# Performance work log

Measured on AMD Instinct MI355X. Metric: run time of the kernel, lower is better.

Reference implementation:

```python
import jax, jax.numpy as jnp
import numpy as np

DEFAULT_MASK_VALUE = -0.7 * float(np.finfo(np.float32).max)


def setup_inputs() -> dict:
    key = jax.random.key(0)
    kq, kk, kv = jax.random.split(key, 3)
    B, S, Hq, Hkv, D = 2, 2048, 16, 8, 128
    return {
        "query": jax.random.normal(kq, (B, S, Hq, D), dtype=jnp.float32),
        "key": jax.random.normal(kk, (B, S, Hkv, D), dtype=jnp.float32),
        "value": jax.random.normal(kv, (B, S, Hkv, D), dtype=jnp.float32),
        "chunk_size": 512,
    }


def reference(query, key, value, chunk_size):
    """Chunked-causal GQA attention (AttentionOp with attention_type='chunk').

    Tokens attend only within their own chunk, causally. This is exactly the
    mask from _generate_chunk_attention_mask, exploited as a block-diagonal
    structure so cross-chunk logits are never materialized.
    """
    B, S, Hq, D = query.shape
    Hkv = key.shape[2]
    G = Hq // Hkv  # GQA group size
    C = int(chunk_size)
    NC = S // C
    scale = 1.0 / np.float32(np.sqrt(D))  # depth scaling (folded into query init in MaxText)

    # float32 qk product / logits (float32_qk_product & float32_logits = True)
    qf = query.astype(jnp.float32).reshape(B, NC, C, Hkv, G, D)
    kf = key.astype(jnp.float32).reshape(B, NC, C, Hkv, D)
    vf = value.reshape(B, NC, C, Hkv, D)

    # per-chunk logits: [B, NC, Hkv, G, C(q), C(k)]
    logits = jnp.einsum("bnqhgd,bnkhd->bnhgqk", qf, kf) * scale

    # causal mask within each chunk (apply_mask_to_logits semantics)
    causal = jnp.arange(C)[:, None] >= jnp.arange(C)[None, :]
    logits = jnp.where(causal, logits, DEFAULT_MASK_VALUE)

    probs = jax.nn.softmax(logits, axis=-1).astype(value.dtype)
    out = jnp.einsum("bnhgqk,bnkhd->bnqhgd", probs, vf)
    return out.reshape(B, S, Hq, D)
```

## Files before the change

kernel.cpp:

```cpp
#include <hip/hip_runtime.h>
#include <hip/hip_bf16.h>

typedef __bf16 bf16;
typedef bf16  bf16x2 __attribute__((ext_vector_type(2)));
typedef bf16  bf16x4 __attribute__((ext_vector_type(4)));
typedef bf16  bf16x8 __attribute__((ext_vector_type(8)));
typedef float f32x4  __attribute__((ext_vector_type(4)));
typedef float f32x16 __attribute__((ext_vector_type(16)));

#define MFMA32(A, B, C) __builtin_amdgcn_mfma_f32_32x32x16_bf16((A), (B), (C), 0, 0, 0)

namespace {
constexpr int   kS = 2048, kHq = 16, kHkv = 8, kD = 128, kChunk = 512;
constexpr int   kNT   = 8;
constexpr int   kStrK = kHkv * kD;
constexpr float kScale = 0.08838834764831845f;
constexpr float kThr   = 8.0f;
}

union U32B { bf16x2 h; unsigned u; };
union PAU  { unsigned u[4]; bf16x8 v; };

__global__ __launch_bounds__(512, 2)
void attn_chunk(const float* __restrict__ Qg, const float* __restrict__ Kg,
                const float* __restrict__ Vg, float* __restrict__ Og) {
  __shared__ __attribute__((aligned(16))) bf16 ldsK[2][64 * 128];
  __shared__ __attribute__((aligned(16))) bf16 ldsV[2][128 * 64];

  const int t = threadIdx.x, lane = t & 63, w = t >> 6;
  const int l31 = lane & 31, hi = lane >> 5;

  const int bid = blockIdx.x;
  const int gid = (bid & 7) * 32 + (bid >> 3);
  const int p = gid & 1, hq = (gid >> 1) & 15, n = (gid >> 5) & 3, b = (gid >> 7) & 1;
  const int h = hq >> 1;

  const int a     = (w < 4) ? (7 - 2 * w) : (2 * w - 8);
  const int need  = a + 1;
  const int strip = 2 * a + p;
  const int qg    = n * kChunk + strip * 32 + l31;
  const int rowoff = 32 * p + l31;

  bf16x8 qf[8];
  {
    const float* qp = Qg + ((size_t)(b * kS + qg) * kHq + hq) * kD;
#pragma unroll
    for (int dk = 0; dk < 8; ++dk) {
      f32x4 x0 = *(const f32x4*)(qp + dk * 16 + 8 * hi);
      f32x4 x1 = *(const f32x4*)(qp + dk * 16 + 8 * hi + 4);
      bf16x8 v;
#pragma unroll
      for (int j = 0; j < 4; ++j) { v[j] = (bf16)(x0[j] * kScale); v[4 + j] = (bf16)(x1[j] * kScale); }
      qf[dk] = v;
    }
  }

  f32x16 o[4];
#pragma unroll
  for (int dt = 0; dt < 4; ++dt)
#pragma unroll
    for (int r = 0; r < 16; ++r) o[dt][r] = 0.f;
  float m = -1e30f, l = 0.f;

  const float* kpz = Kg + ((size_t)(b * kS + n * kChunk) * kHkv + h) * kD;
  const float* vpz = Vg + ((size_t)(b * kS + n * kChunk) * kHkv + h) * kD;

  const int sKey = t >> 5, sD4 = t & 31;
  const int vKp = t & 31, vD4h = t >> 5;

  f32x4 kf[4], va[2], vb[2];
  auto issue = [&](int kt) {
    const float* kp = kpz + (size_t)kt * 64 * kStrK;
    const float* vp = vpz + (size_t)kt * 64 * kStrK;
#pragma unroll
    for (int it = 0; it < 4; ++it)
      kf[it] = *(const f32x4*)(kp + (size_t)(16 * it + sKey) * kStrK + sD4 * 4);
#pragma unroll
    for (int it = 0; it < 2; ++it) {
      va[it] = *(const f32x4*)(vp + (size_t)(2 * vKp) * kStrK + (16 * it + vD4h) * 4);
      vb[it] = *(const f32x4*)(vp + (size_t)(2 * vKp + 1) * kStrK + (16 * it + vD4h) * 4);
    }
  };
  auto stage = [&](int buf) {
#pragma unroll
    for (int it = 0; it < 4; ++it) {
      const int key = 16 * it + sKey;
      bf16x4 kb;
#pragma unroll
      for (int j = 0; j < 4; ++j) kb[j] = (bf16)kf[it][j];
      *(bf16x4*)&ldsK[buf][key * 128 + ((sD4 * 4) ^ ((key & 7) << 3))] = kb;
    }
#pragma unroll
    for (int it = 0; it < 2; ++it) {
#pragma unroll
      for (int j = 0; j < 4; ++j) {
        const int d = (16 * it + vD4h) * 4 + j;
        U32B uu; uu.h = bf16x2{(bf16)va[it][j], (bf16)vb[it][j]};
        *(unsigned*)&ldsV[buf][d * 64 + ((2 * vKp) ^ ((d & 7) << 3))] = uu.u;
      }
    }
  };

  auto compute = [&](int buf, bool diag) {
    f32x16 s[2];
#pragma unroll
    for (int ks = 0; ks < 2; ++ks)
#pragma unroll
      for (int r = 0; r < 16; ++r) s[ks][r] = 0.f;
    __builtin_amdgcn_s_setprio(1);
#pragma unroll
    for (int ks = 0; ks < 2; ++ks) {
      const int key = ks * 32 + l31, swz = (key & 7) << 3;
      const bf16* kb = &ldsK[buf][key * 128];
#pragma unroll
      for (int dk = 0; dk < 8; ++dk) {
        bf16x8 kfr = *(const bf16x8*)&kb[(dk * 16 + 8 * hi) ^ swz];
        s[ks] = MFMA32(kfr, qf[dk], s[ks]);
      }
    }
    __builtin_amdgcn_s_setprio(0);
    if (diag) {
#pragma unroll
      for (int ks = 0; ks < 2; ++ks)
#pragma unroll
        for (int r = 0; r < 16; ++r) {
          const int key = ks * 32 + (r & 3) + 8 * (r >> 2) + 4 * hi;
          if (key > rowoff) s[ks][r] = -1e30f;
        }
    }
    float mx = -1e30f;
#pragma unroll
    for (int ks = 0; ks < 2; ++ks)
#pragma unroll
      for (int r = 0; r < 16; ++r) mx = fmaxf(mx, s[ks][r]);
    mx = fmaxf(mx, __shfl_xor(mx, 32, 64));
    if (__any(mx > m + kThr)) {
      const float mn = fmaxf(m, mx), c = __expf(m - mn);
      l *= c;
#pragma unroll
      for (int dt = 0; dt < 4; ++dt)
#pragma unroll
        for (int r = 0; r < 16; ++r) o[dt][r] *= c;
      m = mn;
    }
    unsigned u[2][8];
    float lp = 0.f;
#pragma unroll
    for (int ks = 0; ks < 2; ++ks)
#pragma unroll
      for (int j = 0; j < 8; ++j) {
        const float p0 = __expf(s[ks][2 * j] - m), p1 = __expf(s[ks][2 * j + 1] - m);
        lp += p0 + p1;
        U32B uu; uu.h = bf16x2{(bf16)p0, (bf16)p1};
        u[ks][j] = uu.u;
      }
    l += lp;
    unsigned rc[2][4];
#pragma unroll
    for (int ks = 0; ks < 2; ++ks)
#pragma unroll
      for (int i = 0; i < 4; ++i)
        rc[ks][i] = (unsigned)__shfl_xor((int)u[ks][(i & 1) + 4 * (i >> 1) + (hi ? 0 : 2)], 32, 64);
    bf16x8 pa[4];
#pragma unroll
    for (int ks = 0; ks < 2; ++ks)
#pragma unroll
      for (int kh = 0; kh < 2; ++kh) {
        PAU pu;
        pu.u[0] = hi ? rc[ks][2 * kh]     : u[ks][4 * kh];
        pu.u[1] = hi ? rc[ks][2 * kh + 1] : u[ks][4 * kh + 1];
        pu.u[2] = hi ? u[ks][4 * kh + 2]  : rc[ks][2 * kh];
        pu.u[3] = hi ? u[ks][4 * kh + 3]  : rc[ks][2 * kh + 1];
        pa[ks * 2 + kh] = pu.v;
      }
    __builtin_amdgcn_s_setprio(1);
#pragma unroll
    for (int dt = 0; dt < 4; ++dt) {
      const int d = dt * 32 + l31, swz = (d & 7) << 3;
      const bf16* vbp = &ldsV[buf][d * 64];
#pragma unroll
      for (int ksl = 0; ksl < 4; ++ksl) {
        bf16x8 vfr = *(const bf16x8*)&vbp[(ksl * 16 + 8 * hi) ^ swz];
        o[dt] = MFMA32(vfr, pa[ksl], o[dt]);
      }
    }
    __builtin_amdgcn_s_setprio(0);
  };

  issue(0);
  stage(0);
  issue(1);
  __syncthreads();
#pragma unroll 1
  for (int kt = 0; kt < kNT; ++kt) {
    if (kt + 1 < kNT) {
      stage((kt + 1) & 1);
      if (kt + 2 < kNT) issue(kt + 2);
    }
    if (kt < need) compute(kt & 1, kt == need - 1);
    if (kt + 1 < kNT) __syncthreads();
  }

  l += __shfl_xor(l, 32, 64);
  const float inv = 1.f / l;
  float* op = Og + ((size_t)(b * kS + qg) * kHq + hq) * kD;
#pragma unroll
  for (int dt = 0; dt < 4; ++dt)
#pragma unroll
    for (int rq = 0; rq < 4; ++rq) {
      f32x4 st;
#pragma unroll
      for (int rr = 0; rr < 4; ++rr) st[rr] = o[dt][4 * rq + rr] * inv;
      *(f32x4*)(op + dt * 32 + 8 * rq + 4 * hi) = st;
    }
}

extern "C" void kernel_launch(void* const* d_in, const int* in_sizes, int n_in,
                              void* d_out, int out_size, void* d_ws, size_t ws_size,
                              hipStream_t stream) {
  (void)in_sizes; (void)n_in; (void)d_ws; (void)ws_size; (void)out_size;
  const float* Q = (const float*)d_in[0];
  const float* K = (const float*)d_in[1];
  const float* V = (const float*)d_in[2];
  float* O = (float*)d_out;
  dim3 grid(256);
  dim3 block(512);
  hipLaunchKernelGGL(attn_chunk, grid, block, 0, stream, Q, K, V, O);
}
```

Baseline: 34.96 us.

## Split chunk work into 4-wave blocks with per-block loop bounds and exp2 softmax

Each block now has 4 waves instead of 8, with twice as many blocks. Strips are paired so each block's K/V loop only runs to the deepest strip it needs (maxNeed), which cuts K/V tile loads for blocks whose strips sit early in the chunk. The log2e factor is folded into the query scale so the softmax can use exp2 directly. The plain barrier is replaced by an explicit lgkmcnt wait plus s_barrier. In exchange, each thread issues twice the K/V loads per tile, and K/V is now loaded by four blocks per chunk and head instead of two.

```diff
diff --git a/kernel.cpp b/kernel.cpp
--- a/kernel.cpp
+++ b/kernel.cpp
@@ -12,16 +12,23 @@
 
 namespace {
 constexpr int   kS = 2048, kHq = 16, kHkv = 8, kD = 128, kChunk = 512;
-constexpr int   kNT   = 8;
-constexpr int   kStrK = kHkv * kD;
-constexpr float kScale = 0.08838834764831845f;
-constexpr float kThr   = 8.0f;
+constexpr int   kStrK  = kHkv * kD;
+constexpr float kLog2e = 1.4426950408889634f;
+constexpr float kScale = 0.08838834764831845f * kLog2e;
+constexpr float kThr   = 8.0f * kLog2e;
 }
 
 union U32B { bf16x2 h; unsigned u; };
 union PAU  { unsigned u[4]; bf16x8 v; };
 
-__global__ __launch_bounds__(512, 2)
+__device__ __forceinline__ void lgkm_barrier() {
+  __builtin_amdgcn_sched_barrier(0);
+  asm volatile("s_waitcnt lgkmcnt(0)" ::: "memory");
+  __builtin_amdgcn_s_barrier();
+  __builtin_amdgcn_sched_barrier(0);
+}
+
+__global__ __launch_bounds__(256, 2)
 void attn_chunk(const float* __restrict__ Qg, const float* __restrict__ Kg,
                 const float* __restrict__ Vg, float* __restrict__ Og) {
   __shared__ __attribute__((aligned(16))) bf16 ldsK[2][64 * 128];
@@ -31,15 +38,15 @@
   const int l31 = lane & 31, hi = lane >> 5;
 
   const int bid = blockIdx.x;
-  const int gid = (bid & 7) * 32 + (bid >> 3);
-  const int p = gid & 1, hq = (gid >> 1) & 15, n = (gid >> 5) & 3, b = (gid >> 7) & 1;
+  const int gid = (bid & 7) * 64 + (bid >> 3);
+  const int j = gid & 3, hq = (gid >> 2) & 15, n = (gid >> 6) & 3, b = (gid >> 8) & 1;
   const int h = hq >> 1;
 
-  const int a     = (w < 4) ? (7 - 2 * w) : (2 * w - 8);
-  const int need  = a + 1;
-  const int strip = 2 * a + p;
-  const int qg    = n * kChunk + strip * 32 + l31;
-  const int rowoff = 32 * p + l31;
+  const int strip   = (w == 0) ? j : (w == 1) ? (15 - j) : (w == 2) ? (7 - j) : (8 + j);
+  const int need    = (strip >> 1) + 1;
+  const int maxNeed = 8 - (j >> 1);
+  const int qg      = n * kChunk + strip * 32 + l31;
+  const int rowoff  = 32 * (strip & 1) + l31;
 
   bf16x8 qf[8];
   {
@@ -50,7 +57,7 @@
       f32x4 x1 = *(const f32x4*)(qp + dk * 16 + 8 * hi + 4);
       bf16x8 v;
 #pragma unroll
-      for (int j = 0; j < 4; ++j) { v[j] = (bf16)(x0[j] * kScale); v[4 + j] = (bf16)(x1[j] * kScale); }
+      for (int q = 0; q < 4; ++q) { v[q] = (bf16)(x0[q] * kScale); v[4 + q] = (bf16)(x1[q] * kScale); }
       qf[dk] = v;
     }
   }
@@ -68,34 +75,34 @@
   const int sKey = t >> 5, sD4 = t & 31;
   const int vKp = t & 31, vD4h = t >> 5;
 
-  f32x4 kf[4], va[2], vb[2];
+  f32x4 kf[8], va[4], vb[4];
   auto issue = [&](int kt) {
     const float* kp = kpz + (size_t)kt * 64 * kStrK;
     const float* vp = vpz + (size_t)kt * 64 * kStrK;
 #pragma unroll
-    for (int it = 0; it < 4; ++it)
-      kf[it] = *(const f32x4*)(kp + (size_t)(16 * it + sKey) * kStrK + sD4 * 4);
-#pragma unroll
-    for (int it = 0; it < 2; ++it) {
-      va[it] = *(const f32x4*)(vp + (size_t)(2 * vKp) * kStrK + (16 * it + vD4h) * 4);
-      vb[it] = *(const f32x4*)(vp + (size_t)(2 * vKp + 1) * kStrK + (16 * it + vD4h) * 4);
+    for (int it = 0; it < 8; ++it)
+      kf[it] = *(const f32x4*)(kp + (size_t)(8 * it + sKey) * kStrK + sD4 * 4);
+#pragma unroll
+    for (int it = 0; it < 4; ++it) {
+      va[it] = *(const f32x4*)(vp + (size_t)(2 * vKp) * kStrK + (8 * it + vD4h) * 4);
+      vb[it] = *(const f32x4*)(vp + (size_t)(2 * vKp + 1) * kStrK + (8 * it + vD4h) * 4);
     }
   };
   auto stage = [&](int buf) {
 #pragma unroll
+    for (int it = 0; it < 8; ++it) {
+      const int key = 8 * it + sKey;
+      bf16x4 kb;
+#pragma unroll
+      for (int q = 0; q < 4; ++q) kb[q] = (bf16)kf[it][q];
+      *(bf16x4*)&ldsK[buf][key * 128 + ((sD4 * 4) ^ ((key & 7) << 3))] = kb;
+    }
+#pragma unroll
     for (int it = 0; it < 4; ++it) {
-      const int key = 16 * it + sKey;
-      bf16x4 kb;
-#pragma unroll
-      for (int j = 0; j < 4; ++j) kb[j] = (bf16)kf[it][j];
-      *(bf16x4*)&ldsK[buf][key * 128 + ((sD4 * 4) ^ ((key & 7) << 3))] = kb;
-    }
-#pragma unroll
-    for (int it = 0; it < 2; ++it) {
-#pragma unroll
-      for (int j = 0; j < 4; ++j) {
-        const int d = (16 * it + vD4h) * 4 + j;
-        U32B uu; uu.h = bf16x2{(bf16)va[it][j], (bf16)vb[it][j]};
+#pragma unroll
+      for (int q = 0; q < 4; ++q) {
+        const int d = (8 * it + vD4h) * 4 + q;
+        U32B uu; uu.h = bf16x2{(bf16)va[it][q], (bf16)vb[it][q]};
         *(unsigned*)&ldsV[buf][d * 64 + ((2 * vKp) ^ ((d & 7) << 3))] = uu.u;
       }
     }
@@ -135,7 +142,7 @@
       for (int r = 0; r < 16; ++r) mx = fmaxf(mx, s[ks][r]);
     mx = fmaxf(mx, __shfl_xor(mx, 32, 64));
     if (__any(mx > m + kThr)) {
-      const float mn = fmaxf(m, mx), c = __expf(m - mn);
+      const float mn = fmaxf(m, mx), c = exp2f(m - mn);
       l *= c;
 #pragma unroll
       for (int dt = 0; dt < 4; ++dt)
@@ -148,11 +155,11 @@
 #pragma unroll
     for (int ks = 0; ks < 2; ++ks)
 #pragma unroll
-      for (int j = 0; j < 8; ++j) {
-        const float p0 = __expf(s[ks][2 * j] - m), p1 = __expf(s[ks][2 * j + 1] - m);
+      for (int q = 0; q < 8; ++q) {
+        const float p0 = exp2f(s[ks][2 * q] - m), p1 = exp2f(s[ks][2 * q + 1] - m);
         lp += p0 + p1;
         U32B uu; uu.h = bf16x2{(bf16)p0, (bf16)p1};
-        u[ks][j] = uu.u;
+        u[ks][q] = uu.u;
       }
     l += lp;
     unsigned rc[2][4];
@@ -190,15 +197,15 @@
   issue(0);
   stage(0);
   issue(1);
-  __syncthreads();
+  lgkm_barrier();
 #pragma unroll 1
-  for (int kt = 0; kt < kNT; ++kt) {
-    if (kt + 1 < kNT) {
+  for (int kt = 0; kt < maxNeed; ++kt) {
+    if (kt + 1 < maxNeed) {
       stage((kt + 1) & 1);
-      if (kt + 2 < kNT) issue(kt + 2);
-    }
-    if (kt < need) compute(kt & 1, kt == need - 1);
-    if (kt + 1 < kNT) __syncthreads();
+      if (kt + 2 < maxNeed) issue(kt + 2);
+    }
+    if (kt < need) compute(kt & 1, kt + 1 == need);
+    if (kt + 1 < maxNeed) lgkm_barrier();
   }
 
   l += __shfl_xor(l, 32, 64);
@@ -223,7 +230,7 @@
   const float* K = (const float*)d_in[1];
   const float* V = (const float*)d_in[2];
   float* O = (float*)d_out;
-  dim3 grid(256);
-  dim3 block(512);
+  dim3 grid(512);
+  dim3 block(256);
   hipLaunchKernelGGL(attn_chunk, grid, block, 0, stream, Q, K, V, O);
 }
```

New measurement: 45.54 us. +30.2%, slower.

## Prepack K/V to bf16 MFMA-fragment layout in workspace, stream from global

Applied to the files above, without the earlier changes.

Adds a prepack kernel that converts K and V to bf16 once per call and writes them in a tiled layout matching the MFMA fragment order. The attention kernel then reads fragments straight from global/L2 without LDS staging or barriers, and skips tiles beyond its causal limit. This removes redundant fp32 loads and conversions done by every query-head block, at the cost of a second launch and a workspace round trip. The softmax also switches to exp2 with log2e folded into the scale, and an LDS-based fallback kernel runs when the workspace is too small.

```diff
diff --git a/kernel.cpp b/kernel.cpp
--- a/kernel.cpp
+++ b/kernel.cpp
@@ -12,21 +12,70 @@
 
 namespace {
 constexpr int   kS = 2048, kHq = 16, kHkv = 8, kD = 128, kChunk = 512;
-constexpr int   kNT   = 8;
-constexpr int   kStrK = kHkv * kD;
-constexpr float kScale = 0.08838834764831845f;
-constexpr float kThr   = 8.0f;
+constexpr int   kStrK  = kHkv * kD;
+constexpr float kLog2e = 1.4426950408889634f;
+constexpr float kScale = 0.08838834764831845f * kLog2e;
+constexpr float kThr   = 8.0f * kLog2e;
+constexpr size_t kWsNeed = 512ull * 8192 * 2 * 2;
 }
 
 union U32B { bf16x2 h; unsigned u; };
 union PAU  { unsigned u[4]; bf16x8 v; };
 
+__global__ __launch_bounds__(256, 4)
+void prepack(const float* __restrict__ Kg, const float* __restrict__ Vg,
+             bf16* __restrict__ Kws, bf16* __restrict__ Vws) {
+  __shared__ __attribute__((aligned(16))) bf16 img[8192];
+  const int t  = threadIdx.x;
+  const int bk = blockIdx.x;
+  const int kt = bk & 7, h = (bk >> 3) & 7, n = (bk >> 6) & 3, b = bk >> 8;
+  const size_t rowbase = ((size_t)(b * kS + n * kChunk + kt * 64) * kHkv + h) * kD;
+
+  const float* kp = Kg + rowbase;
+#pragma unroll
+  for (int it = 0; it < 8; ++it) {
+    const int idx = it * 256 + t, key = idx >> 5, d4 = idx & 31;
+    f32x4 v = *(const f32x4*)(kp + (size_t)key * kStrK + d4 * 4);
+#pragma unroll
+    for (int j = 0; j < 4; ++j) {
+      const int d = d4 * 4 + j;
+      img[(((((key >> 5) * 8 + (d >> 4)) * 2 + ((d >> 3) & 1)) << 8) +
+           ((key & 31) << 3) + (d & 7))] = (bf16)v[j];
+    }
+  }
+  __syncthreads();
+  {
+    bf16* dst = Kws + (size_t)bk * 8192;
+#pragma unroll
+    for (int i = 0; i < 4; ++i)
+      *(bf16x8*)(dst + t * 8 + i * 2048) = *(const bf16x8*)(&img[t * 8 + i * 2048]);
+  }
+  __syncthreads();
+
+  const float* vp = Vg + rowbase;
+#pragma unroll
+  for (int it = 0; it < 8; ++it) {
+    const int idx = it * 256 + t, key = idx >> 5, d4 = idx & 31;
+    f32x4 v = *(const f32x4*)(vp + (size_t)key * kStrK + d4 * 4);
+#pragma unroll
+    for (int j = 0; j < 4; ++j) {
+      const int d = d4 * 4 + j;
+      img[(((((d >> 5) * 4 + (key >> 4)) * 2 + ((key >> 3) & 1)) << 8) +
+           ((d & 31) << 3) + (key & 7))] = (bf16)v[j];
+    }
+  }
+  __syncthreads();
+  {
+    bf16* dst = Vws + (size_t)bk * 8192;
+#pragma unroll
+    for (int i = 0; i < 4; ++i)
+      *(bf16x8*)(dst + t * 8 + i * 2048) = *(const bf16x8*)(&img[t * 8 + i * 2048]);
+  }
+}
+
 __global__ __launch_bounds__(512, 2)
-void attn_chunk(const float* __restrict__ Qg, const float* __restrict__ Kg,
-                const float* __restrict__ Vg, float* __restrict__ Og) {
-  __shared__ __attribute__((aligned(16))) bf16 ldsK[2][64 * 128];
-  __shared__ __attribute__((aligned(16))) bf16 ldsV[2][128 * 64];
-
+void attn_stream(const float* __restrict__ Qg, const bf16* __restrict__ Kws,
+                 const bf16* __restrict__ Vws, float* __restrict__ Og) {
   const int t = threadIdx.x, lane = t & 63, w = t >> 6;
   const int l31 = lane & 31, hi = lane >> 5;
 
@@ -35,10 +84,10 @@
   const int p = gid & 1, hq = (gid >> 1) & 15, n = (gid >> 5) & 3, b = (gid >> 7) & 1;
   const int h = hq >> 1;
 
-  const int a     = (w < 4) ? (7 - 2 * w) : (2 * w - 8);
-  const int need  = a + 1;
-  const int strip = 2 * a + p;
-  const int qg    = n * kChunk + strip * 32 + l31;
+  const int a      = (w < 4) ? (7 - 2 * w) : (2 * w - 8);
+  const int need   = a + 1;
+  const int strip  = 2 * a + p;
+  const int qg     = n * kChunk + strip * 32 + l31;
   const int rowoff = 32 * p + l31;
 
   bf16x8 qf[8];
@@ -50,7 +99,7 @@
       f32x4 x1 = *(const f32x4*)(qp + dk * 16 + 8 * hi + 4);
       bf16x8 v;
 #pragma unroll
-      for (int j = 0; j < 4; ++j) { v[j] = (bf16)(x0[j] * kScale); v[4 + j] = (bf16)(x1[j] * kScale); }
+      for (int q = 0; q < 4; ++q) { v[q] = (bf16)(x0[q] * kScale); v[4 + q] = (bf16)(x1[q] * kScale); }
       qf[dk] = v;
     }
   }
@@ -62,46 +111,15 @@
     for (int r = 0; r < 16; ++r) o[dt][r] = 0.f;
   float m = -1e30f, l = 0.f;
 
-  const float* kpz = Kg + ((size_t)(b * kS + n * kChunk) * kHkv + h) * kD;
-  const float* vpz = Vg + ((size_t)(b * kS + n * kChunk) * kHkv + h) * kD;
-
-  const int sKey = t >> 5, sD4 = t & 31;
-  const int vKp = t & 31, vD4h = t >> 5;
-
-  f32x4 kf[4], va[2], vb[2];
-  auto issue = [&](int kt) {
-    const float* kp = kpz + (size_t)kt * 64 * kStrK;
-    const float* vp = vpz + (size_t)kt * 64 * kStrK;
-#pragma unroll
-    for (int it = 0; it < 4; ++it)
-      kf[it] = *(const f32x4*)(kp + (size_t)(16 * it + sKey) * kStrK + sD4 * 4);
-#pragma unroll
-    for (int it = 0; it < 2; ++it) {
-      va[it] = *(const f32x4*)(vp + (size_t)(2 * vKp) * kStrK + (16 * it + vD4h) * 4);
-      vb[it] = *(const f32x4*)(vp + (size_t)(2 * vKp + 1) * kStrK + (16 * it + vD4h) * 4);
-    }
-  };
-  auto stage = [&](int buf) {
-#pragma unroll
-    for (int it = 0; it < 4; ++it) {
-      const int key = 16 * it + sKey;
-      bf16x4 kb;
-#pragma unroll
-      for (int j = 0; j < 4; ++j) kb[j] = (bf16)kf[it][j];
-      *(bf16x4*)&ldsK[buf][key * 128 + ((sD4 * 4) ^ ((key & 7) << 3))] = kb;
-    }
-#pragma unroll
-    for (int it = 0; it < 2; ++it) {
-#pragma unroll
-      for (int j = 0; j < 4; ++j) {
-        const int d = (16 * it + vD4h) * 4 + j;
-        U32B uu; uu.h = bf16x2{(bf16)va[it][j], (bf16)vb[it][j]};
-        *(unsigned*)&ldsV[buf][d * 64 + ((2 * vKp) ^ ((d & 7) << 3))] = uu.u;
-      }
-    }
-  };
-
-  auto compute = [&](int buf, bool diag) {
+  const bf16* kt0 = Kws + ((size_t)((b * 4 + n) * 8 + h)) * 8 * 8192;
+  const bf16* vt0 = Vws + ((size_t)((b * 4 + n) * 8 + h)) * 8 * 8192;
+
+#pragma unroll 1
+  for (int kt = 0; kt < need; ++kt) {
+    const bf16* ktile = kt0 + (size_t)kt * 8192;
+    const bf16* vtile = vt0 + (size_t)kt * 8192;
+    const bool  diag  = (kt + 1 == need);
+
     f32x16 s[2];
 #pragma unroll
     for (int ks = 0; ks < 2; ++ks)
@@ -110,15 +128,14 @@
     __builtin_amdgcn_s_setprio(1);
 #pragma unroll
     for (int ks = 0; ks < 2; ++ks) {
-      const int key = ks * 32 + l31, swz = (key & 7) << 3;
-      const bf16* kb = &ldsK[buf][key * 128];
 #pragma unroll
       for (int dk = 0; dk < 8; ++dk) {
-        bf16x8 kfr = *(const bf16x8*)&kb[(dk * 16 + 8 * hi) ^ swz];
+        bf16x8 kfr = *(const bf16x8*)(ktile + ((((ks * 8 + dk) * 2 + hi) * 32 + l31) * 8));
         s[ks] = MFMA32(kfr, qf[dk], s[ks]);
       }
     }
     __builtin_amdgcn_s_setprio(0);
+
     if (diag) {
 #pragma unroll
       for (int ks = 0; ks < 2; ++ks)
@@ -135,7 +152,7 @@
       for (int r = 0; r < 16; ++r) mx = fmaxf(mx, s[ks][r]);
     mx = fmaxf(mx, __shfl_xor(mx, 32, 64));
     if (__any(mx > m + kThr)) {
-      const float mn = fmaxf(m, mx), c = __expf(m - mn);
+      const float mn = fmaxf(m, mx), c = exp2f(m - mn);
       l *= c;
 #pragma unroll
       for (int dt = 0; dt < 4; ++dt)
@@ -148,11 +165,11 @@
 #pragma unroll
     for (int ks = 0; ks < 2; ++ks)
 #pragma unroll
-      for (int j = 0; j < 8; ++j) {
-        const float p0 = __expf(s[ks][2 * j] - m), p1 = __expf(s[ks][2 * j + 1] - m);
+      for (int q = 0; q < 8; ++q) {
+        const float p0 = exp2f(s[ks][2 * q] - m), p1 = exp2f(s[ks][2 * q + 1] - m);
         lp += p0 + p1;
         U32B uu; uu.h = bf16x2{(bf16)p0, (bf16)p1};
-        u[ks][j] = uu.u;
+        u[ks][q] = uu.u;
       }
     l += lp;
     unsigned rc[2][4];
@@ -176,6 +193,175 @@
     __builtin_amdgcn_s_setprio(1);
 #pragma unroll
     for (int dt = 0; dt < 4; ++dt) {
+#pragma unroll
+      for (int ksl = 0; ksl < 4; ++ksl) {
+        bf16x8 vfr = *(const bf16x8*)(vtile + ((((dt * 4 + ksl) * 2 + hi) * 32 + l31) * 8));
+        o[dt] = MFMA32(vfr, pa[ksl], o[dt]);
+      }
+    }
+    __builtin_amdgcn_s_setprio(0);
+  }
+
+  l += __shfl_xor(l, 32, 64);
+  const float inv = 1.f / l;
+  float* op = Og + ((size_t)(b * kS + qg) * kHq + hq) * kD;
+#pragma unroll
+  for (int dt = 0; dt < 4; ++dt)
+#pragma unroll
+    for (int rq = 0; rq < 4; ++rq) {
+      f32x4 st;
+#pragma unroll
+      for (int rr = 0; rr < 4; ++rr) st[rr] = o[dt][4 * rq + rr] * inv;
+      *(f32x4*)(op + dt * 32 + 8 * rq + 4 * hi) = st;
+    }
+}
+
+__global__ __launch_bounds__(512, 2)
+void attn_fb(const float* __restrict__ Qg, const float* __restrict__ Kg,
+             const float* __restrict__ Vg, float* __restrict__ Og) {
+  __shared__ __attribute__((aligned(16))) bf16 ldsK[2][64 * 128];
+  __shared__ __attribute__((aligned(16))) bf16 ldsV[2][128 * 64];
+
+  const int t = threadIdx.x, lane = t & 63, w = t >> 6;
+  const int l31 = lane & 31, hi = lane >> 5;
+  const int bid = blockIdx.x;
+  const int gid = (bid & 7) * 32 + (bid >> 3);
+  const int p = gid & 1, hq = (gid >> 1) & 15, n = (gid >> 5) & 3, b = (gid >> 7) & 1;
+  const int h = hq >> 1;
+  const int a = (w < 4) ? (7 - 2 * w) : (2 * w - 8);
+  const int need = a + 1, strip = 2 * a + p;
+  const int qg = n * kChunk + strip * 32 + l31;
+  const int rowoff = 32 * p + l31;
+
+  bf16x8 qf[8];
+  {
+    const float* qp = Qg + ((size_t)(b * kS + qg) * kHq + hq) * kD;
+#pragma unroll
+    for (int dk = 0; dk < 8; ++dk) {
+      f32x4 x0 = *(const f32x4*)(qp + dk * 16 + 8 * hi);
+      f32x4 x1 = *(const f32x4*)(qp + dk * 16 + 8 * hi + 4);
+      bf16x8 v;
+#pragma unroll
+      for (int q = 0; q < 4; ++q) { v[q] = (bf16)(x0[q] * kScale); v[4 + q] = (bf16)(x1[q] * kScale); }
+      qf[dk] = v;
+    }
+  }
+  f32x16 o[4];
+#pragma unroll
+  for (int dt = 0; dt < 4; ++dt)
+#pragma unroll
+    for (int r = 0; r < 16; ++r) o[dt][r] = 0.f;
+  float m = -1e30f, l = 0.f;
+
+  const float* kpz = Kg + ((size_t)(b * kS + n * kChunk) * kHkv + h) * kD;
+  const float* vpz = Vg + ((size_t)(b * kS + n * kChunk) * kHkv + h) * kD;
+  const int sKey = t >> 5, sD4 = t & 31;
+  const int vKp = t & 31, vD4h = t >> 5;
+
+  f32x4 kf[4], va[2], vb[2];
+  auto issue = [&](int kt) {
+    const float* kp = kpz + (size_t)kt * 64 * kStrK;
+    const float* vp = vpz + (size_t)kt * 64 * kStrK;
+#pragma unroll
+    for (int it = 0; it < 4; ++it)
+      kf[it] = *(const f32x4*)(kp + (size_t)(16 * it + sKey) * kStrK + sD4 * 4);
+#pragma unroll
+    for (int it = 0; it < 2; ++it) {
+      va[it] = *(const f32x4*)(vp + (size_t)(2 * vKp) * kStrK + (16 * it + vD4h) * 4);
+      vb[it] = *(const f32x4*)(vp + (size_t)(2 * vKp + 1) * kStrK + (16 * it + vD4h) * 4);
+    }
+  };
+  auto stage = [&](int buf) {
+#pragma unroll
+    for (int it = 0; it < 4; ++it) {
+      const int key = 16 * it + sKey;
+      bf16x4 kb;
+#pragma unroll
+      for (int q = 0; q < 4; ++q) kb[q] = (bf16)kf[it][q];
+      *(bf16x4*)&ldsK[buf][key * 128 + ((sD4 * 4) ^ ((key & 7) << 3))] = kb;
+    }
+#pragma unroll
+    for (int it = 0; it < 2; ++it) {
+#pragma unroll
+      for (int q = 0; q < 4; ++q) {
+        const int d = (16 * it + vD4h) * 4 + q;
+        U32B uu; uu.h = bf16x2{(bf16)va[it][q], (bf16)vb[it][q]};
+        *(unsigned*)&ldsV[buf][d * 64 + ((2 * vKp) ^ ((d & 7) << 3))] = uu.u;
+      }
+    }
+  };
+  auto compute = [&](int buf, bool diag) {
+    f32x16 s[2];
+#pragma unroll
+    for (int ks = 0; ks < 2; ++ks)
+#pragma unroll
+      for (int r = 0; r < 16; ++r) s[ks][r] = 0.f;
+#pragma unroll
+    for (int ks = 0; ks < 2; ++ks) {
+      const int key = ks * 32 + l31, swz = (key & 7) << 3;
+      const bf16* kb = &ldsK[buf][key * 128];
+#pragma unroll
+      for (int dk = 0; dk < 8; ++dk) {
+        bf16x8 kfr = *(const bf16x8*)&kb[(dk * 16 + 8 * hi) ^ swz];
+        s[ks] = MFMA32(kfr, qf[dk], s[ks]);
+      }
+    }
+    if (diag) {
+#pragma unroll
+      for (int ks = 0; ks < 2; ++ks)
+#pragma unroll
+        for (int r = 0; r < 16; ++r) {
+          const int key = ks * 32 + (r & 3) + 8 * (r >> 2) + 4 * hi;
+          if (key > rowoff) s[ks][r] = -1e30f;
+        }
+    }
+    float mx = -1e30f;
+#pragma unroll
+    for (int ks = 0; ks < 2; ++ks)
+#pragma unroll
+      for (int r = 0; r < 16; ++r) mx = fmaxf(mx, s[ks][r]);
+    mx = fmaxf(mx, __shfl_xor(mx, 32, 64));
+    if (__any(mx > m + kThr)) {
+      const float mn = fmaxf(m, mx), c = exp2f(m - mn);
+      l *= c;
+#pragma unroll
+      for (int dt = 0; dt < 4; ++dt)
+#pragma unroll
+        for (int r = 0; r < 16; ++r) o[dt][r] *= c;
+      m = mn;
+    }
+    unsigned u[2][8];
+    float lp = 0.f;
+#pragma unroll
+    for (int ks = 0; ks < 2; ++ks)
+#pragma unroll
+      for (int q = 0; q < 8; ++q) {
+        const float p0 = exp2f(s[ks][2 * q] - m), p1 = exp2f(s[ks][2 * q + 1] - m);
+        lp += p0 + p1;
+        U32B uu; uu.h = bf16x2{(bf16)p0, (bf16)p1};
+        u[ks][q] = uu.u;
+      }
+    l += lp;
+    unsigned rc[2][4];
+#pragma unroll
+    for (int ks = 0; ks < 2; ++ks)
+#pragma unroll
+      for (int i = 0; i < 4; ++i)
+        rc[ks][i] = (unsigned)__shfl_xor((int)u[ks][(i & 1) + 4 * (i >> 1) + (hi ? 0 : 2)], 32, 64);
+    bf16x8 pa[4];
+#pragma unroll
+    for (int ks = 0; ks < 2; ++ks)
+#pragma unroll
+      for (int kh = 0; kh < 2; ++kh) {
+        PAU pu;
+        pu.u[0] = hi ? rc[ks][2 * kh]     : u[ks][4 * kh];
+        pu.u[1] = hi ? rc[ks][2 * kh + 1] : u[ks][4 * kh + 1];
+        pu.u[2] = hi ? u[ks][4 * kh + 2]  : rc[ks][2 * kh];
+        pu.u[3] = hi ? u[ks][4 * kh + 3]  : rc[ks][2 * kh + 1];
+        pa[ks * 2 + kh] = pu.v;
+      }
+#pragma unroll
+    for (int dt = 0; dt < 4; ++dt) {
       const int d = dt * 32 + l31, swz = (d & 7) << 3;
       const bf16* vbp = &ldsV[buf][d * 64];
 #pragma unroll
@@ -184,21 +370,18 @@
         o[dt] = MFMA32(vfr, pa[ksl], o[dt]);
       }
     }
-    __builtin_amdgcn_s_setprio(0);
   };
 
-  issue(0);
-  stage(0);
-  issue(1);
+  issue(0); stage(0); issue(1);
   __syncthreads();
 #pragma unroll 1
-  for (int kt = 0; kt < kNT; ++kt) {
-    if (kt + 1 < kNT) {
+  for (int kt = 0; kt < 8; ++kt) {
+    if (kt + 1 < 8) {
       stage((kt + 1) & 1);
-      if (kt + 2 < kNT) issue(kt + 2);
-    }
-    if (kt < need) compute(kt & 1, kt == need - 1);
-    if (kt + 1 < kNT) __syncthreads();
+      if (kt + 2 < 8) issue(kt + 2);
+    }
+    if (kt < need) compute(kt & 1, kt + 1 == need);
+    if (kt + 1 < 8) __syncthreads();
   }
 
   l += __shfl_xor(l, 32, 64);
@@ -218,12 +401,17 @@
 extern "C" void kernel_launch(void* const* d_in, const int* in_sizes, int n_in,
                               void* d_out, int out_size, void* d_ws, size_t ws_size,
                               hipStream_t stream) {
-  (void)in_sizes; (void)n_in; (void)d_ws; (void)ws_size; (void)out_size;
+  (void)in_sizes; (void)n_in; (void)out_size;
   const float* Q = (const float*)d_in[0];
   const float* K = (const float*)d_in[1];
   const float* V = (const float*)d_in[2];
   float* O = (float*)d_out;
-  dim3 grid(256);
-  dim3 block(512);
-  hipLaunchKernelGGL(attn_chunk, grid, block, 0, stream, Q, K, V, O);
+  if (ws_size >= kWsNeed) {
+    bf16* Kws = (bf16*)d_ws;
+    bf16* Vws = Kws + 512ull * 8192;
+    hipLaunchKernelGGL(prepack, dim3(512), dim3(256), 0, stream, K, V, Kws, Vws);
+    hipLaunchKernelGGL(attn_stream, dim3(256), dim3(512), 0, stream, Q, Kws, Vws, O);
+  } else {
+    hipLaunchKernelGGL(attn_fb, dim3(256), dim3(512), 0, stream, Q, K, V, O);
+  }
 }
```

After: 84.34 us. 2.41x slower.
